# Kernel optimization log

Hardware: AMD Instinct MI355X
Metric: run time of the kernel (lower is better)

## Reference

```python
import jax, jax.numpy as jnp
import numpy as np

B, N, C = 2, 8192, 768
H, K = 12, 256
D = C // H
HID = 4 * C
EPS = 1e-6

def layer_norm(x, w, b):
    mu = jnp.mean(x, axis=-1, keepdims=True)
    var = jnp.mean(jnp.square(x - mu), axis=-1, keepdims=True)
    return (x - mu) * jax.lax.rsqrt(var + EPS) * w + b

def setup_inputs() -> dict:
    key = jax.random.key(0)
    ks = jax.random.split(key, 8)
    s = 0.02
    return {
        "x": jax.random.normal(ks[0], (B, N, C), jnp.float32),
        "ln1_w": jnp.ones((C,), jnp.float32),
        "ln1_b": jnp.zeros((C,), jnp.float32),
        "qkv_w": jax.random.normal(ks[1], (C, 3 * C), jnp.float32) * s,
        "qkv_b": jnp.zeros((3 * C,), jnp.float32),
        "Ek": jax.random.normal(ks[2], (N, K), jnp.float32) * s,
        "Ev": jax.random.normal(ks[3], (N, K), jnp.float32) * s,
        "proj_w": jax.random.normal(ks[4], (C, C), jnp.float32) * s,
        "proj_b": jnp.zeros((C,), jnp.float32),
        "ln2_w": jnp.ones((C,), jnp.float32),
        "ln2_b": jnp.zeros((C,), jnp.float32),
        "fc1_w": jax.random.normal(ks[5], (C, HID), jnp.float32) * s,
        "fc1_b": jnp.zeros((HID,), jnp.float32),
        "fc2_w": jax.random.normal(ks[6], (HID, C), jnp.float32) * s,
        "fc2_b": jnp.zeros((C,), jnp.float32),
    }

def reference(x, ln1_w, ln1_b, qkv_w, qkv_b, Ek, Ev, proj_w, proj_b,
              ln2_w, ln2_b, fc1_w, fc1_b, fc2_w, fc2_b):
    scale = D ** -0.5
    # --- attention branch ---
    h = layer_norm(x, ln1_w, ln1_b)
    qkv = h @ qkv_w + qkv_b                      # (B,N,3C)
    qkv = qkv.reshape(B, N, 3, H, D).transpose(2, 0, 3, 1, 4)  # (3,B,H,N,D)
    q, k, v = qkv[0], qkv[1], qkv[2]
    # Linformer: project K/V along sequence dim N -> K
    k_proj = jnp.einsum('bhnd,nk->bhkd', k, Ek)
    v_proj = jnp.einsum('bhnd,nk->bhkd', v, Ev)
    logits = jnp.einsum('bhnd,bhkd->bhnk', q, k_proj) * scale
    logits = jnp.clip(logits, -50.0, 50.0)
    attn = jax.nn.softmax(logits, axis=-1)
    o = jnp.einsum('bhnk,bhkd->bhnd', attn, v_proj)
    o = o.transpose(0, 2, 1, 3).reshape(B, N, C)
    o = o @ proj_w + proj_b
    x = x + o                                    # alpha_attn = 1.0
    # --- MLP branch ---
    h = layer_norm(x, ln2_w, ln2_b)
    h = jax.nn.gelu(h @ fc1_w + fc1_b, approximate=False)
    h = h @ fc2_w + fc2_b
    return x + h                                 # alpha_mlp = 1.0
```

## Files before the change

### kernel.cpp

```cpp
#include <hip/hip_runtime.h>
#include <cstdint>

#define DEV __device__ __forceinline__

typedef __bf16 bf16x8 __attribute__((ext_vector_type(8)));
typedef float f32x4 __attribute__((ext_vector_type(4)));

DEV uint16_t f2bf(float f) {
  uint32_t u = __float_as_uint(f);
  u += 0x7FFFu + ((u >> 16) & 1u);
  return (uint16_t)(u >> 16);
}
DEV float bf2f(uint16_t h) { return __uint_as_float(((uint32_t)h) << 16); }

DEV void gload16(const void* g, void* l) {
  __builtin_amdgcn_global_load_lds((const __attribute__((address_space(1))) void*)g,
                                   (__attribute__((address_space(3))) void*)l, 16, 0, 0);
}

template <int N> DEV void waitcnt_vm() {
  if constexpr (N == 0) asm volatile("s_waitcnt vmcnt(0)" ::: "memory");
  else if constexpr (N == 4) asm volatile("s_waitcnt vmcnt(4)" ::: "memory");
  else static_assert(N == 0 || N == 4, "unsupported vmcnt");
}

DEV float gelu_f(float v) {
  float u = v * (0.7978845608f + 0.0356774081f * v * v);
  return v / (1.f + __expf(-2.f * u));
}

__global__ __launch_bounds__(256) void ln768(const float* __restrict__ x,
                                             const float* __restrict__ w,
                                             const float* __restrict__ b,
                                             uint16_t* __restrict__ out) {
  const size_t row = blockIdx.x;
  const float* xr = x + row * 768;
  const int t = threadIdx.x;
  float v0 = xr[t], v1 = xr[t + 256], v2 = xr[t + 512];
  float s = v0 + v1 + v2;
  float s2 = v0 * v0 + v1 * v1 + v2 * v2;
#pragma unroll
  for (int o = 32; o; o >>= 1) {
    s += __shfl_down(s, o);
    s2 += __shfl_down(s2, o);
  }
  __shared__ float sh[8];
  if ((t & 63) == 0) { sh[t >> 6] = s; sh[4 + (t >> 6)] = s2; }
  __syncthreads();
  s = sh[0] + sh[1] + sh[2] + sh[3];
  s2 = sh[4] + sh[5] + sh[6] + sh[7];
  const float mu = s * (1.f / 768.f);
  const float var = s2 * (1.f / 768.f) - mu * mu;
  const float rstd = rsqrtf(var + 1e-6f);
  uint16_t* orow = out + row * 768;
  orow[t]       = f2bf((v0 - mu) * rstd * w[t] + b[t]);
  orow[t + 256] = f2bf((v1 - mu) * rstd * w[t + 256] + b[t + 256]);
  orow[t + 512] = f2bf((v2 - mu) * rstd * w[t + 512] + b[t + 512]);
}

__global__ __launch_bounds__(256) void transpose_f2b(const float* __restrict__ in,
                                                     uint16_t* __restrict__ outp,
                                                     int ldin, int ldout) {
  __shared__ float tile[32][33];
  const int tx = threadIdx.x, ty = threadIdx.y;
  const size_t x = (size_t)blockIdx.x * 32 + tx;
  const size_t y = (size_t)blockIdx.y * 32 + ty;
#pragma unroll
  for (int j = 0; j < 4; ++j) tile[ty + j * 8][tx] = in[(y + j * 8) * ldin + x];
  __syncthreads();
  const size_t x2 = (size_t)blockIdx.y * 32 + tx;
  const size_t y2 = (size_t)blockIdx.x * 32 + ty;
#pragma unroll
  for (int j = 0; j < 4; ++j) outp[(y2 + j * 8) * ldout + x2] = f2bf(tile[tx][ty + j * 8]);
}

__global__ __launch_bounds__(256) void transpose_b2b(const uint16_t* __restrict__ in,
                                                     uint16_t* __restrict__ outp,
                                                     int ldin, int ldout) {
  __shared__ uint16_t tile[32][33];
  const int tx = threadIdx.x, ty = threadIdx.y;
  const size_t x = (size_t)blockIdx.x * 32 + tx;
  const size_t y = (size_t)blockIdx.y * 32 + ty;
#pragma unroll
  for (int j = 0; j < 4; ++j) tile[ty + j * 8][tx] = in[(y + j * 8) * ldin + x];
  __syncthreads();
  const size_t x2 = (size_t)blockIdx.y * 32 + tx;
  const size_t y2 = (size_t)blockIdx.x * 32 + ty;
#pragma unroll
  for (int j = 0; j < 4; ++j) outp[(y2 + j * 8) * ldout + x2] = tile[tx][ty + j * 8];
}

__global__ __launch_bounds__(256) void kv_tn(const uint16_t* __restrict__ EkT,
                                             const uint16_t* __restrict__ EvT,
                                             const uint16_t* __restrict__ qkv,
                                             float* __restrict__ part) {
  const int bid = blockIdx.x;
  const int wg = (bid & 7) * 96 + (bid >> 3);
  const int inner = wg & 15;
  const int kt = inner & 3, ns = inner >> 2;
  const int rest = wg >> 4;
  const int ct = rest % 12, kvb = rest / 12;
  const int kv = kvb >> 1, b = kvb & 1;
  const int k0 = kt * 64, c0 = ct * 64, nsb = ns * 2048;

  const uint16_t* E = kv ? EvT : EkT;
  const uint16_t* KV = qkv + (size_t)b * 8192 * 2304 + 768 + kv * 768 + c0;
  const int tid = threadIdx.x, wave = tid >> 6, lane = tid & 63;
  const int l16 = lane & 15, lhi = lane >> 4;
  const int wm = wave >> 1, wn = wave & 1;

  f32x4 acc[2][2];
#pragma unroll
  for (int m = 0; m < 2; ++m)
#pragma unroll
    for (int n = 0; n < 2; ++n) acc[m][n] = f32x4{0.f, 0.f, 0.f, 0.f};

  const uint16_t* Eb = E + (size_t)(k0 + wm * 32 + l16) * 8192 + nsb + lhi * 8;
  const uint16_t* KVb = KV + ((size_t)nsb + lhi * 8) * 2304 + wn * 32 + l16;

  for (int n0 = 0; n0 < 2048; n0 += 32) {
    bf16x8 ef[2];
    ef[0] = *(const bf16x8*)(Eb + n0);
    ef[1] = *(const bf16x8*)(Eb + 16 * 8192 + n0);
    bf16x8 vf[2];
#pragma unroll
    for (int nf = 0; nf < 2; ++nf) {
      const uint16_t* p = KVb + (size_t)n0 * 2304 + nf * 16;
      union { bf16x8 v; uint16_t u[8]; } tu;
#pragma unroll
      for (int j = 0; j < 8; ++j) tu.u[j] = p[(size_t)j * 2304];
      vf[nf] = tu.v;
    }
#pragma unroll
    for (int m = 0; m < 2; ++m)
#pragma unroll
      for (int nf = 0; nf < 2; ++nf)
        acc[m][nf] = __builtin_amdgcn_mfma_f32_16x16x32_bf16(ef[m], vf[nf], acc[m][nf], 0, 0, 0);
  }

  float* outp = part + ((size_t)ns * 4 + kvb) * 196608;
#pragma unroll
  for (int m = 0; m < 2; ++m)
#pragma unroll
    for (int nf = 0; nf < 2; ++nf)
#pragma unroll
      for (int r = 0; r < 4; ++r)
        outp[(size_t)(k0 + wm * 32 + m * 16 + lhi * 4 + r) * 768 + c0 + wn * 32 + nf * 16 + l16] =
            acc[m][nf][r];
}

__global__ __launch_bounds__(256) void kv_reduce(const float* __restrict__ part,
                                                 uint16_t* __restrict__ kproj) {
  const int kvb = blockIdx.y;
  const int i = blockIdx.x * 256 + threadIdx.x;
  const float* p = part + (size_t)kvb * 196608 + i;
  float s = p[0] + p[786432] + p[2 * 786432] + p[3 * 786432];
  kproj[(size_t)kvb * 196608 + i] = f2bf(s);
}

__global__ __launch_bounds__(256, 3) void attn_fused(
    const uint16_t* __restrict__ qkv, const uint16_t* __restrict__ kproj,
    const uint16_t* __restrict__ vprojT, uint16_t* __restrict__ o) {
  const int bh = blockIdx.y;
  const int b = bh / 12, h = bh % 12;
  const int n0 = blockIdx.x * 64;
  const int tid = threadIdx.x, wave = tid >> 6, lane = tid & 63;
  const int l16 = lane & 15, lhi = lane >> 4;
  const int wm = wave >> 1, wn = wave & 1;

  __shared__ __align__(16) uint16_t sP[64 * 256];
  __shared__ float redm[2][64], reds[2][64], recs[64];

  const uint16_t* Kp = kproj + (size_t)b * 196608 + h * 64;
  const uint16_t* Qp = qkv + ((size_t)b * 8192 + n0) * 2304 + h * 64;
  const uint16_t* Vp = vprojT + ((size_t)b * 768 + h * 64) * 256;

  f32x4 st[8][2];
#pragma unroll
  for (int m = 0; m < 8; ++m)
#pragma unroll
    for (int nf = 0; nf < 2; ++nf) st[m][nf] = f32x4{0.f, 0.f, 0.f, 0.f};
#pragma unroll
  for (int ks = 0; ks < 2; ++ks) {
    bf16x8 kf[8], qf[2];
#pragma unroll
    for (int m = 0; m < 8; ++m) {
      const int kvi = wm * 128 + m * 16 + l16;
      kf[m] = *(const bf16x8*)(Kp + (size_t)kvi * 768 + ks * 32 + lhi * 8);
    }
#pragma unroll
    for (int nf = 0; nf < 2; ++nf) {
      const int n = wn * 32 + nf * 16 + l16;
      qf[nf] = *(const bf16x8*)(Qp + (size_t)n * 2304 + ks * 32 + lhi * 8);
    }
#pragma unroll
    for (int m = 0; m < 8; ++m)
#pragma unroll
      for (int nf = 0; nf < 2; ++nf)
        st[m][nf] = __builtin_amdgcn_mfma_f32_16x16x32_bf16(kf[m], qf[nf], st[m][nf], 0, 0, 0);
  }

  float pmax[2] = {-50.f, -50.f};
#pragma unroll
  for (int m = 0; m < 8; ++m)
#pragma unroll
    for (int nf = 0; nf < 2; ++nf)
#pragma unroll
      for (int r = 0; r < 4; ++r) {
        float v = fminf(fmaxf(st[m][nf][r] * 0.125f, -50.f), 50.f);
        st[m][nf][r] = v;
        pmax[nf] = fmaxf(pmax[nf], v);
      }
#pragma unroll
  for (int nf = 0; nf < 2; ++nf) {
    pmax[nf] = fmaxf(pmax[nf], __shfl_xor(pmax[nf], 16));
    pmax[nf] = fmaxf(pmax[nf], __shfl_xor(pmax[nf], 32));
  }
  if (lhi == 0) {
#pragma unroll
    for (int nf = 0; nf < 2; ++nf) redm[wm][wn * 32 + nf * 16 + l16] = pmax[nf];
  }
  __syncthreads();
  float M[2];
#pragma unroll
  for (int nf = 0; nf < 2; ++nf) {
    const int col = wn * 32 + nf * 16 + l16;
    M[nf] = fmaxf(redm[0][col], redm[1][col]);
  }

  float psum[2] = {0.f, 0.f};
#pragma unroll
  for (int m = 0; m < 8; ++m) {
#pragma unroll
    for (int nf = 0; nf < 2; ++nf) {
      float e0 = __expf(st[m][nf][0] - M[nf]);
      float e1 = __expf(st[m][nf][1] - M[nf]);
      float e2 = __expf(st[m][nf][2] - M[nf]);
      float e3 = __expf(st[m][nf][3] - M[nf]);
      psum[nf] += (e0 + e1) + (e2 + e3);
      uint2 pk;
      pk.x = (uint32_t)f2bf(e0) | ((uint32_t)f2bf(e1) << 16);
      pk.y = (uint32_t)f2bf(e2) | ((uint32_t)f2bf(e3) << 16);
      const int n = wn * 32 + nf * 16 + l16;
      const int kvb2 = (wm * 128 + m * 16 + lhi * 4) * 2;
      *(uint2*)((char*)sP + n * 512 + (kvb2 ^ ((n & 7) << 4))) = pk;
    }
  }
#pragma unroll
  for (int nf = 0; nf < 2; ++nf) {
    psum[nf] += __shfl_xor(psum[nf], 16);
    psum[nf] += __shfl_xor(psum[nf], 32);
  }
  if (lhi == 0) {
#pragma unroll
    for (int nf = 0; nf < 2; ++nf) reds[wm][wn * 32 + nf * 16 + l16] = psum[nf];
  }
  __syncthreads();
  if (wm == 0 && lhi == 0) {
#pragma unroll
    for (int nf = 0; nf < 2; ++nf) {
      const int col = wn * 32 + nf * 16 + l16;
      recs[col] = 1.f / (reds[0][col] + reds[1][col]);
    }
  }
  __syncthreads();

  f32x4 pacc[2][2];
#pragma unroll
  for (int mf = 0; mf < 2; ++mf)
#pragma unroll
    for (int nf = 0; nf < 2; ++nf) pacc[mf][nf] = f32x4{0.f, 0.f, 0.f, 0.f};
#pragma unroll
  for (int ks = 0; ks < 8; ++ks) {
    bf16x8 pa[2], vb[2];
#pragma unroll
    for (int mf = 0; mf < 2; ++mf) {
      const int n = wm * 32 + mf * 16 + l16;
      pa[mf] = *(const bf16x8*)((char*)sP + n * 512 + ((ks * 64 + lhi * 16) ^ ((n & 7) << 4)));
    }
#pragma unroll
    for (int nf = 0; nf < 2; ++nf) {
      const int d = wn * 32 + nf * 16 + l16;
      vb[nf] = *(const bf16x8*)(Vp + (size_t)d * 256 + ks * 32 + lhi * 8);
    }
#pragma unroll
    for (int mf = 0; mf < 2; ++mf)
#pragma unroll
      for (int nf = 0; nf < 2; ++nf)
        pacc[mf][nf] = __builtin_amdgcn_mfma_f32_16x16x32_bf16(pa[mf], vb[nf], pacc[mf][nf], 0, 0, 0);
  }
  uint16_t* orow = o + ((size_t)b * 8192 + n0) * 768 + h * 64;
#pragma unroll
  for (int mf = 0; mf < 2; ++mf) {
#pragma unroll
    for (int r = 0; r < 4; ++r) {
      const int n = wm * 32 + mf * 16 + lhi * 4 + r;
      const float inv = recs[n];
#pragma unroll
      for (int nf = 0; nf < 2; ++nf) {
        const int d = wn * 32 + nf * 16 + l16;
        orow[(size_t)n * 768 + d] = f2bf(pacc[mf][nf][r] * inv);
      }
    }
  }
}

template <bool OUTBF, bool HASBIAS, bool DOGELU, bool HASRES>
__global__ __launch_bounds__(512, 2) void gemm256(
    const uint16_t* __restrict__ A, const uint16_t* __restrict__ B,
    void* __restrict__ Cbase, const float* __restrict__ bias,
    const float* __restrict__ res, int Kd, int lda, int ldb, int ldc) {
  constexpr int PLANE = 8192;
  constexpr int BUF = 4 * PLANE;
  __shared__ __align__(16) uint16_t lds[2 * BUF];

  const int nn = gridDim.y;
  const int nwg = gridDim.x * gridDim.y;
  const int bid = blockIdx.y * gridDim.x + blockIdx.x;
  const int q = nwg >> 3, r8 = nwg & 7, xcd = bid & 7, idx = bid >> 3;
  const int wg = (xcd < r8 ? xcd * (q + 1) : r8 * (q + 1) + (xcd - r8) * q) + idx;
  const int bm = wg / nn, bn = wg % nn;
  const int row0 = bm * 256, col0 = bn * 256;

  const int tid = threadIdx.x;
  const int wave = tid >> 6, lane = tid & 63;
  const int wm = wave >> 2, wn = wave & 3;
  const int l16 = lane & 15, lhi = lane >> 4;
  const int srow = tid >> 2, sq = tid & 3;

  auto stage = [&](int b, int t, int op, int kh) {
    const int k0 = t * 64 + kh * 32;
    const uint16_t* G = op ? B : A;
    const int ld = op ? ldb : lda;
    const int r0 = op ? col0 : row0;
    uint16_t* dst = lds + b * BUF + op * 2 * PLANE + kh * PLANE;
#pragma unroll
    for (int j = 0; j < 2; ++j) {
      const int rw = j * 128 + srow;
      const int sl = sq ^ ((rw >> 1) & 3);
      gload16(G + (size_t)(r0 + rw) * ld + k0 + sl * 8, dst + rw * 32 + sq * 8);
    }
  };
  auto rdA = [&](const uint16_t* buf, int ks, int mh, int m) -> bf16x8 {
    const int rw = wm * 128 + mh * 64 + m * 16 + l16;
    const int sl = lhi ^ ((rw >> 1) & 3);
    return *(const bf16x8*)(buf + ks * PLANE + rw * 32 + sl * 8);
  };
  auto rdB = [&](const uint16_t* buf, int ks, int n) -> bf16x8 {
    const int rw = wn * 64 + n * 16 + l16;
    const int sl = lhi ^ ((rw >> 1) & 3);
    return *(const bf16x8*)(buf + 2 * PLANE + ks * PLANE + rw * 32 + sl * 8);
  };

  f32x4 acc[8][4];
#pragma unroll
  for (int m = 0; m < 8; ++m)
#pragma unroll
    for (int n = 0; n < 4; ++n) acc[m][n] = f32x4{0.f, 0.f, 0.f, 0.f};

  const int NT = Kd >> 6;
  stage(0, 0, 0, 0); stage(0, 0, 1, 0); stage(0, 0, 0, 1); stage(0, 0, 1, 1);
  waitcnt_vm<4>();
  __builtin_amdgcn_s_barrier();
  asm volatile("" ::: "memory");

  for (int u = 0; u < NT; ++u) {
    const uint16_t* cb = lds + (u & 1) * BUF;
    const int nb = (u + 1) & 1;
    const bool st = (u + 1) < NT;
    bf16x8 bfr[4], afr[4];
#pragma unroll
    for (int ks = 0; ks < 2; ++ks) {
#pragma unroll
      for (int mh = 0; mh < 2; ++mh) {
        if (mh == 0) {
#pragma unroll
          for (int n = 0; n < 4; ++n) bfr[n] = rdB(cb, ks, n);
        }
#pragma unroll
        for (int m = 0; m < 4; ++m) afr[m] = rdA(cb, ks, mh, m);
        if (st) stage(nb, u + 1, mh, ks);
        __builtin_amdgcn_s_barrier();
        asm volatile("" ::: "memory");
        __builtin_amdgcn_s_setprio(1);
#pragma unroll
        for (int m = 0; m < 4; ++m)
#pragma unroll
          for (int n = 0; n < 4; ++n)
            acc[mh * 4 + m][n] =
                __builtin_amdgcn_mfma_f32_16x16x32_bf16(afr[m], bfr[n], acc[mh * 4 + m][n], 0, 0, 0);
        __builtin_amdgcn_s_setprio(0);
        if (mh == 1) {
          if (st) waitcnt_vm<4>();
          else waitcnt_vm<0>();
        }
        __builtin_amdgcn_s_barrier();
        asm volatile("" ::: "memory");
      }
    }
  }

  float* Cf = (float*)Cbase;
  uint16_t* Cb = (uint16_t*)Cbase;
#pragma unroll
  for (int m = 0; m < 8; ++m) {
#pragma unroll
    for (int n = 0; n < 4; ++n) {
      const int col = col0 + wn * 64 + n * 16 + l16;
      float bv = 0.f;
      if (HASBIAS) bv = bias[col];
#pragma unroll
      for (int r = 0; r < 4; ++r) {
        const int row = row0 + wm * 128 + m * 16 + lhi * 4 + r;
        float v = acc[m][n][r] + bv;
        if (DOGELU) v = gelu_f(v);
        const size_t cidx = (size_t)row * ldc + col;
        if (HASRES) v += res[cidx];
        if (OUTBF) Cb[cidx] = f2bf(v);
        else Cf[cidx] = v;
      }
    }
  }
}

extern "C" void kernel_launch(void* const* d_in, const int* in_sizes, int n_in,
                              void* d_out, int out_size, void* d_ws, size_t ws_size,
                              hipStream_t stream) {
  const float* x      = (const float*)d_in[0];
  const float* ln1_w  = (const float*)d_in[1];
  const float* ln1_b  = (const float*)d_in[2];
  const float* qkv_w  = (const float*)d_in[3];
  const float* qkv_b  = (const float*)d_in[4];
  const float* Ek     = (const float*)d_in[5];
  const float* Ev     = (const float*)d_in[6];
  const float* proj_w = (const float*)d_in[7];
  const float* proj_b = (const float*)d_in[8];
  const float* ln2_w  = (const float*)d_in[9];
  const float* ln2_b  = (const float*)d_in[10];
  const float* fc1_w  = (const float*)d_in[11];
  const float* fc1_b  = (const float*)d_in[12];
  const float* fc2_w  = (const float*)d_in[13];
  const float* fc2_b  = (const float*)d_in[14];
  float* out = (float*)d_out;

  char* w8 = (char*)d_ws;
  size_t off = 0;
  auto take = [&](size_t bytes) { char* p = w8 + off; off += bytes; return p; };
  uint16_t* qkv_wT  = (uint16_t*)take(2304ull * 768 * 2);
  uint16_t* proj_wT = (uint16_t*)take(768ull * 768 * 2);
  uint16_t* fc1_wT  = (uint16_t*)take(3072ull * 768 * 2);
  uint16_t* fc2_wT  = (uint16_t*)take(768ull * 3072 * 2);
  uint16_t* EkT     = (uint16_t*)take(256ull * 8192 * 2);
  uint16_t* EvT     = (uint16_t*)take(256ull * 8192 * 2);
  uint16_t* h_bf    = (uint16_t*)take(16384ull * 768 * 2);
  uint16_t* qkv_bf  = (uint16_t*)take(16384ull * 2304 * 2);
  uint16_t* big     = (uint16_t*)take(100663296ull);
  uint16_t* kproj   = (uint16_t*)take(2ull * 2 * 256 * 768 * 2);
  uint16_t* vprojT  = (uint16_t*)take(2ull * 768 * 256 * 2);
  uint16_t* o_bf    = (uint16_t*)take(16384ull * 768 * 2);
  float* part = (float*)big;
  (void)ws_size; (void)in_sizes; (void)n_in; (void)out_size;

  const dim3 tb(32, 8);
  transpose_f2b<<<dim3(72, 24), tb, 0, stream>>>(qkv_w, qkv_wT, 2304, 768);
  transpose_f2b<<<dim3(24, 24), tb, 0, stream>>>(proj_w, proj_wT, 768, 768);
  transpose_f2b<<<dim3(96, 24), tb, 0, stream>>>(fc1_w, fc1_wT, 3072, 768);
  transpose_f2b<<<dim3(24, 96), tb, 0, stream>>>(fc2_w, fc2_wT, 768, 3072);
  transpose_f2b<<<dim3(8, 256), tb, 0, stream>>>(Ek, EkT, 256, 8192);
  transpose_f2b<<<dim3(8, 256), tb, 0, stream>>>(Ev, EvT, 256, 8192);
  ln768<<<16384, 256, 0, stream>>>(x, ln1_w, ln1_b, h_bf);
  gemm256<true, true, false, false><<<dim3(64, 9), 512, 0, stream>>>(
      h_bf, qkv_wT, qkv_bf, qkv_b, nullptr, 768, 768, 768, 2304);
  kv_tn<<<768, 256, 0, stream>>>(EkT, EvT, qkv_bf, part);
  kv_reduce<<<dim3(768, 4), 256, 0, stream>>>(part, kproj);
  for (int b = 0; b < 2; ++b)
    transpose_b2b<<<dim3(24, 8), tb, 0, stream>>>(
        kproj + (size_t)(2 + b) * 196608, vprojT + (size_t)b * 768 * 256, 768, 256);
  attn_fused<<<dim3(128, 24), 256, 0, stream>>>(qkv_bf, kproj, vprojT, o_bf);
  gemm256<false, true, false, true><<<dim3(64, 3), 512, 0, stream>>>(
      o_bf, proj_wT, out, proj_b, x, 768, 768, 768, 768);
  ln768<<<16384, 256, 0, stream>>>(out, ln2_w, ln2_b, h_bf);
  gemm256<true, true, true, false><<<dim3(64, 12), 512, 0, stream>>>(
      h_bf, fc1_wT, big, fc1_b, nullptr, 768, 768, 768, 3072);
  gemm256<false, true, false, true><<<dim3(64, 3), 512, 0, stream>>>(
      big, fc2_wT, out, fc2_b, out, 3072, 3072, 3072, 768);
}
```

Measured before the change: 524.5 us.

## Replace 256x256 GEMM with 128x128 tiles and triple-buffered K pipeline

Replaces the 256x256-tile, 512-thread GEMM with a 128x128-tile, 256-thread kernel that steps K in 32-wide slices through a three-stage LDS ring, using one barrier per step instead of several. Smaller tiles give more workgroups (e.g. 768 instead of 192 for the proj/fc2 GEMMs), which should fill the 256 CUs better and allow three blocks per CU. The trade-off is lower arithmetic intensity per tile, so each operand is read from global memory more often.

```diff
diff --git a/kernel.cpp b/kernel.cpp
--- a/kernel.cpp
+++ b/kernel.cpp
@@ -306,13 +306,12 @@
 }
 
 template <bool OUTBF, bool HASBIAS, bool DOGELU, bool HASRES>
-__global__ __launch_bounds__(512, 2) void gemm256(
+__global__ __launch_bounds__(256, 3) void gemm128(
     const uint16_t* __restrict__ A, const uint16_t* __restrict__ B,
     void* __restrict__ Cbase, const float* __restrict__ bias,
     const float* __restrict__ res, int Kd, int lda, int ldb, int ldc) {
-  constexpr int PLANE = 8192;
-  constexpr int BUF = 4 * PLANE;
-  __shared__ __align__(16) uint16_t lds[2 * BUF];
+  constexpr int PL = 4096;
+  __shared__ __align__(16) uint16_t lds[3 * 2 * PL];
 
   const int nn = gridDim.y;
   const int nwg = gridDim.x * gridDim.y;
@@ -320,90 +319,74 @@
   const int q = nwg >> 3, r8 = nwg & 7, xcd = bid & 7, idx = bid >> 3;
   const int wg = (xcd < r8 ? xcd * (q + 1) : r8 * (q + 1) + (xcd - r8) * q) + idx;
   const int bm = wg / nn, bn = wg % nn;
-  const int row0 = bm * 256, col0 = bn * 256;
+  const int row0 = bm * 128, col0 = bn * 128;
 
   const int tid = threadIdx.x;
   const int wave = tid >> 6, lane = tid & 63;
-  const int wm = wave >> 2, wn = wave & 3;
+  const int wm = wave >> 1, wn = wave & 1;
   const int l16 = lane & 15, lhi = lane >> 4;
   const int srow = tid >> 2, sq = tid & 3;
 
-  auto stage = [&](int b, int t, int op, int kh) {
-    const int k0 = t * 64 + kh * 32;
-    const uint16_t* G = op ? B : A;
-    const int ld = op ? ldb : lda;
-    const int r0 = op ? col0 : row0;
-    uint16_t* dst = lds + b * BUF + op * 2 * PLANE + kh * PLANE;
+  auto stage = [&](int buf, int t) {
+    const int k0 = t * 32;
+    uint16_t* sa = lds + buf * 2 * PL;
 #pragma unroll
     for (int j = 0; j < 2; ++j) {
-      const int rw = j * 128 + srow;
+      const int rw = j * 64 + srow;
       const int sl = sq ^ ((rw >> 1) & 3);
-      gload16(G + (size_t)(r0 + rw) * ld + k0 + sl * 8, dst + rw * 32 + sq * 8);
+      gload16(A + (size_t)(row0 + rw) * lda + k0 + sl * 8, sa + rw * 32 + sq * 8);
+    }
+#pragma unroll
+    for (int j = 0; j < 2; ++j) {
+      const int rw = j * 64 + srow;
+      const int sl = sq ^ ((rw >> 1) & 3);
+      gload16(B + (size_t)(col0 + rw) * ldb + k0 + sl * 8, sa + PL + rw * 32 + sq * 8);
     }
   };
-  auto rdA = [&](const uint16_t* buf, int ks, int mh, int m) -> bf16x8 {
-    const int rw = wm * 128 + mh * 64 + m * 16 + l16;
-    const int sl = lhi ^ ((rw >> 1) & 3);
-    return *(const bf16x8*)(buf + ks * PLANE + rw * 32 + sl * 8);
-  };
-  auto rdB = [&](const uint16_t* buf, int ks, int n) -> bf16x8 {
-    const int rw = wn * 64 + n * 16 + l16;
-    const int sl = lhi ^ ((rw >> 1) & 3);
-    return *(const bf16x8*)(buf + 2 * PLANE + ks * PLANE + rw * 32 + sl * 8);
-  };
-
-  f32x4 acc[8][4];
-#pragma unroll
-  for (int m = 0; m < 8; ++m)
+
+  f32x4 acc[4][4];
+#pragma unroll
+  for (int m = 0; m < 4; ++m)
 #pragma unroll
     for (int n = 0; n < 4; ++n) acc[m][n] = f32x4{0.f, 0.f, 0.f, 0.f};
 
-  const int NT = Kd >> 6;
-  stage(0, 0, 0, 0); stage(0, 0, 1, 0); stage(0, 0, 0, 1); stage(0, 0, 1, 1);
-  waitcnt_vm<4>();
-  __builtin_amdgcn_s_barrier();
-  asm volatile("" ::: "memory");
-
-  for (int u = 0; u < NT; ++u) {
-    const uint16_t* cb = lds + (u & 1) * BUF;
-    const int nb = (u + 1) & 1;
-    const bool st = (u + 1) < NT;
-    bf16x8 bfr[4], afr[4];
-#pragma unroll
-    for (int ks = 0; ks < 2; ++ks) {
-#pragma unroll
-      for (int mh = 0; mh < 2; ++mh) {
-        if (mh == 0) {
-#pragma unroll
-          for (int n = 0; n < 4; ++n) bfr[n] = rdB(cb, ks, n);
-        }
-#pragma unroll
-        for (int m = 0; m < 4; ++m) afr[m] = rdA(cb, ks, mh, m);
-        if (st) stage(nb, u + 1, mh, ks);
-        __builtin_amdgcn_s_barrier();
-        asm volatile("" ::: "memory");
-        __builtin_amdgcn_s_setprio(1);
-#pragma unroll
-        for (int m = 0; m < 4; ++m)
-#pragma unroll
-          for (int n = 0; n < 4; ++n)
-            acc[mh * 4 + m][n] =
-                __builtin_amdgcn_mfma_f32_16x16x32_bf16(afr[m], bfr[n], acc[mh * 4 + m][n], 0, 0, 0);
-        __builtin_amdgcn_s_setprio(0);
-        if (mh == 1) {
-          if (st) waitcnt_vm<4>();
-          else waitcnt_vm<0>();
-        }
-        __builtin_amdgcn_s_barrier();
-        asm volatile("" ::: "memory");
-      }
-    }
+  const int NT = Kd >> 5;
+  stage(0, 0);
+  stage(1, 1);
+
+  for (int t = 0; t < NT; ++t) {
+    if (t < NT - 1) waitcnt_vm<4>();
+    else waitcnt_vm<0>();
+    __builtin_amdgcn_s_barrier();
+    asm volatile("" ::: "memory");
+    if (t + 2 < NT) stage((t + 2) % 3, t + 2);
+
+    const uint16_t* sa = lds + (t % 3) * 2 * PL;
+    const uint16_t* sb = sa + PL;
+    bf16x8 af[4], bfv[4];
+#pragma unroll
+    for (int n = 0; n < 4; ++n) {
+      const int rw = wn * 64 + n * 16 + l16;
+      bfv[n] = *(const bf16x8*)(sb + rw * 32 + (lhi ^ ((rw >> 1) & 3)) * 8);
+    }
+#pragma unroll
+    for (int m = 0; m < 4; ++m) {
+      const int rw = wm * 64 + m * 16 + l16;
+      af[m] = *(const bf16x8*)(sa + rw * 32 + (lhi ^ ((rw >> 1) & 3)) * 8);
+    }
+    __builtin_amdgcn_s_setprio(1);
+#pragma unroll
+    for (int m = 0; m < 4; ++m)
+#pragma unroll
+      for (int n = 0; n < 4; ++n)
+        acc[m][n] = __builtin_amdgcn_mfma_f32_16x16x32_bf16(af[m], bfv[n], acc[m][n], 0, 0, 0);
+    __builtin_amdgcn_s_setprio(0);
   }
 
   float* Cf = (float*)Cbase;
   uint16_t* Cb = (uint16_t*)Cbase;
 #pragma unroll
-  for (int m = 0; m < 8; ++m) {
+  for (int m = 0; m < 4; ++m) {
 #pragma unroll
     for (int n = 0; n < 4; ++n) {
       const int col = col0 + wn * 64 + n * 16 + l16;
@@ -411,7 +394,7 @@
       if (HASBIAS) bv = bias[col];
 #pragma unroll
       for (int r = 0; r < 4; ++r) {
-        const int row = row0 + wm * 128 + m * 16 + lhi * 4 + r;
+        const int row = row0 + wm * 64 + m * 16 + lhi * 4 + r;
         float v = acc[m][n][r] + bv;
         if (DOGELU) v = gelu_f(v);
         const size_t cidx = (size_t)row * ldc + col;
@@ -469,7 +452,7 @@
   transpose_f2b<<<dim3(8, 256), tb, 0, stream>>>(Ek, EkT, 256, 8192);
   transpose_f2b<<<dim3(8, 256), tb, 0, stream>>>(Ev, EvT, 256, 8192);
   ln768<<<16384, 256, 0, stream>>>(x, ln1_w, ln1_b, h_bf);
-  gemm256<true, true, false, false><<<dim3(64, 9), 512, 0, stream>>>(
+  gemm128<true, true, false, false><<<dim3(128, 18), 256, 0, stream>>>(
       h_bf, qkv_wT, qkv_bf, qkv_b, nullptr, 768, 768, 768, 2304);
   kv_tn<<<768, 256, 0, stream>>>(EkT, EvT, qkv_bf, part);
   kv_reduce<<<dim3(768, 4), 256, 0, stream>>>(part, kproj);
@@ -477,11 +460,11 @@
     transpose_b2b<<<dim3(24, 8), tb, 0, stream>>>(
         kproj + (size_t)(2 + b) * 196608, vprojT + (size_t)b * 768 * 256, 768, 256);
   attn_fused<<<dim3(128, 24), 256, 0, stream>>>(qkv_bf, kproj, vprojT, o_bf);
-  gemm256<false, true, false, true><<<dim3(64, 3), 512, 0, stream>>>(
+  gemm128<false, true, false, true><<<dim3(128, 6), 256, 0, stream>>>(
       o_bf, proj_wT, out, proj_b, x, 768, 768, 768, 768);
   ln768<<<16384, 256, 0, stream>>>(out, ln2_w, ln2_b, h_bf);
-  gemm256<true, true, true, false><<<dim3(64, 12), 512, 0, stream>>>(
+  gemm128<true, true, true, false><<<dim3(128, 24), 256, 0, stream>>>(
       h_bf, fc1_wT, big, fc1_b, nullptr, 768, 768, 768, 3072);
-  gemm256<false, true, false, true><<<dim3(64, 3), 512, 0, stream>>>(
+  gemm128<false, true, false, true><<<dim3(128, 6), 256, 0, stream>>>(
       big, fc2_wT, out, fc2_b, out, 3072, 3072, 3072, 768);
 }
```

Measured after the change: 514.0 us. 1.02x faster.
